# Kernel optimization log

Measured on AMD Instinct MI355X. Metric: run time of the kernel, lower is better.

Reference implementation:

```python
import jax, jax.numpy as jnp
import numpy as np

RESO = 64
VSIZE = 0.3
VOXEL = VSIZE / RESO
HALF = VOXEL / 2.0


def _voxel_xyz():
    line = (np.arange(RESO, dtype=np.float32) * VOXEL + HALF)
    x, y, z = np.meshgrid(line, line, line, indexing='ij')
    return jnp.asarray(np.stack([x, y, z]))  # [3,R,R,R]


def _grid_sample_2d(feats, gx, gy):
    # feats: [NV,C,H,W]; gx,gy: [NV,N] normalized coords (torch align_corners-style)
    NV, C, H, W = feats.shape
    ix = (gx + 1.0) * 0.5 * (W - 1)
    iy = (gy + 1.0) * 0.5 * (H - 1)
    ix0 = jnp.floor(ix); iy0 = jnp.floor(iy)
    ix1 = ix0 + 1.0;     iy1 = iy0 + 1.0
    # bilinear weights from unclamped corners
    w_nw = (ix1 - ix) * (iy1 - iy)
    w_ne = (ix - ix0) * (iy1 - iy)
    w_sw = (ix1 - ix) * (iy - iy0)
    w_se = (ix - ix0) * (iy - iy0)
    mask = ((ix >= 0) & (ix <= W - 1) & (iy >= 0) & (iy <= H - 1)).astype(feats.dtype)
    cx0 = jnp.clip(ix0, 0, W - 1).astype(jnp.int32)
    cx1 = jnp.clip(ix1, 0, W - 1).astype(jnp.int32)
    cy0 = jnp.clip(iy0, 0, H - 1).astype(jnp.int32)
    cy1 = jnp.clip(iy1, 0, H - 1).astype(jnp.int32)
    feats_flat = feats.reshape(NV, C, H * W)  # [NV,C,HW]
    gather = jax.vmap(lambda f, i: f[:, i])   # per-view [C,HW],[N] -> [C,N]
    v_nw = gather(feats_flat, cy0 * W + cx0)
    v_ne = gather(feats_flat, cy0 * W + cx1)
    v_sw = gather(feats_flat, cy1 * W + cx0)
    v_se = gather(feats_flat, cy1 * W + cx1)
    out = (v_nw * w_nw[:, None] + v_ne * w_ne[:, None]
           + v_sw * w_sw[:, None] + v_se * w_se[:, None])  # [NV,C,N]
    return out, mask


def setup_inputs() -> dict:
    key = jax.random.key(0)
    k_feat, k1, k2, k3 = jax.random.split(key, 4)
    NV, C, H, W = 8, 32, 128, 128
    feats = jax.random.normal(k_feat, (NV, C, H, W), dtype=jnp.float32)
    # realistic pinhole intrinsics for a 512x512 image
    K = np.array([[400.0, 0.0, 256.0], [0.0, 400.0, 256.0], [0.0, 0.0, 1.0]], np.float32)
    Ks = jnp.asarray(np.tile(K, (NV, 1, 1)))
    # identity-rotation w2c poses, camera ~0.5m from volume along +z
    poses = []
    for i in range(NV):
        t = np.array([0.02 * (i - 3.5), 0.01 * (i % 2), 0.5 + 0.02 * i], np.float32)
        poses.append(np.concatenate([np.eye(3, dtype=np.float32), t[:, None]], axis=1))
    ref_poses = jnp.asarray(np.stack(poses))
    bbox = jnp.asarray(np.array([[-0.15, -0.15, 0.0], [0.15, 0.15, 0.3]], np.float32))
    W1 = jax.random.normal(k1, (32, 32), dtype=jnp.float32) * 0.1
    W2 = jax.random.normal(k2, (32, 16), dtype=jnp.float32) * 0.1
    W3 = jax.random.normal(k3, (16, 8), dtype=jnp.float32) * 0.1
    return {"feats": feats, "ref_poses": ref_poses, "Ks": Ks, "bbox": bbox,
            "img_h": 512, "img_w": 512,
            "W1": W1, "b1": jnp.zeros((32,), jnp.float32),
            "W2": W2, "b2": jnp.zeros((16,), jnp.float32),
            "W3": W3, "b3": jnp.zeros((8,), jnp.float32)}


def reference(feats, ref_poses, Ks, bbox, img_h, img_w, W1, b1, W2, b2, W3, b3):
    NV, C, H, W = feats.shape
    dt = feats.dtype
    # homogeneous pad of poses and intrinsics
    pose_h = jnp.tile(jnp.eye(4, dtype=dt), (NV, 1, 1)).at[:, :3, :4].set(ref_poses)
    K_pad = jnp.tile(jnp.eye(4, dtype=dt), (NV, 1, 1)).at[:, :3, :3].set(Ks)
    w2pixel = K_pad @ pose_h  # [NV,4,4]
    # voxel centers in world frame
    xyz = _voxel_xyz() + bbox[0][:, None, None, None]  # [3,R,R,R]
    pts = xyz.reshape(3, -1)                            # [3,N], N=R^3
    homo = jnp.concatenate([pts, jnp.ones_like(pts[0:1])], axis=0)  # [4,N]
    pix = jnp.einsum('vij,jn->vin', w2pixel, homo)[:, :3]           # [NV,3,N]
    z = pix[:, 2]                                                    # [NV,N]
    mask_valid_depth = (z > 0).astype(dt)
    uv = pix[:, :2] / z[:, None, :]                                  # [NV,2,N]
    normalizer = jnp.array([img_w, img_h], dtype=dt)
    grid = uv.transpose(0, 2, 1) / normalizer - 1.0                  # [NV,N,2]
    feat, mask = _grid_sample_2d(feats, grid[..., 0], grid[..., 1])  # [NV,C,N],[NV,N]
    mask = mask * mask_valid_depth
    # [NV,C,(X Y Z)] -> [NV,X,Y,Z,C]
    feat = feat.transpose(0, 2, 1).reshape(NV, RESO, RESO, RESO, C)
    mask = mask.reshape(NV, RESO, RESO, RESO)
    # NOTE: original normalizes over dim=1 (NumX), replicated faithfully
    weight = mask / (jnp.sum(mask, axis=1, keepdims=True) + 1e-8)
    weight = weight[..., None]  # [NV,R,R,R,1]
    h1 = jax.nn.relu(feat @ W1 + b1)
    h2 = jax.nn.relu(h1 @ W2 + b2)
    comp = h2 @ W3 + b3  # [NV,R,R,R,8]
    mean = jnp.sum(comp * weight, axis=0, keepdims=True)
    var = jnp.sum(weight * (comp - mean) ** 2, axis=0, keepdims=True)
    mv = jnp.concatenate([mean, var], axis=-1)       # [1,R,R,R,16]
    return jnp.transpose(mv, (0, 4, 3, 2, 1))        # [1,16,Z,Y,X]
```

## Files before the change

### kernel.cpp

```cpp
#include <hip/hip_runtime.h>
#include <math.h>

#define NVIEW 8
#define CIN   32
#define HF    128
#define WF    128
#define C1    32
#define C2    16
#define C3    8
#define RESO  64
#define PLANE (HF*WF)

typedef _Float16 half8_t  __attribute__((ext_vector_type(8)));
typedef _Float16 half2_t  __attribute__((ext_vector_type(2)));
typedef float    floatx4  __attribute__((ext_vector_type(4)));

static __device__ __forceinline__ float vox_coord(int idx, float b) {
    const float VOXEL = (float)(0.3 / 64.0);
    const float HALFV = (float)(0.3 / 128.0);
    return (float)idx * VOXEL + HALFV + b;
}

static __device__ __forceinline__ void wave_lds_sync() {
    asm volatile("s_waitcnt lgkmcnt(0)" ::: "memory");
}

__global__ void __launch_bounds__(256) k_g(const float* __restrict__ feats,
                                           const float* __restrict__ W1,
                                           const float* __restrict__ b1,
                                           uint4* __restrict__ Gh,
                                           const float* __restrict__ Ks,
                                           const float* __restrict__ poses,
                                           const int* __restrict__ ihp,
                                           const int* __restrict__ iwp,
                                           const float* __restrict__ W2,
                                           const float* __restrict__ b2,
                                           const float* __restrict__ W3,
                                           const float* __restrict__ b3,
                                           float* __restrict__ mats,
                                           _Float16* __restrict__ w2f,
                                           _Float16* __restrict__ w3f,
                                           float* __restrict__ b2f,
                                           float* __restrict__ b3f) {
    if (blockIdx.x == 512) {
        int t = threadIdx.x;
        if (t < NVIEW * 12) {
            int v = t / 12, rc = t % 12, r = rc / 4, c = rc % 4;
            const float* K = Ks + v * 9;
            const float* P = poses + v * 12;
            float s = K[r*3+0]*P[0*4+c] + K[r*3+1]*P[1*4+c] + K[r*3+2]*P[2*4+c];
            float sc = (r == 0) ? 63.5f / (float)iwp[0]
                     : (r == 1) ? 63.5f / (float)ihp[0] : 1.0f;
            mats[v*12 + r*4 + c] = s * sc;
        }
        if (t < 64) {
            int n = t & 15, g = t >> 4;
#pragma unroll
            for (int jj = 0; jj < 8; jj++) {
                int kk = 8 * g + jj;
                w2f[t*8 + jj] = (_Float16)W2[kk * C2 + n];
                float w3v = (kk < C2 && n < C3) ? W3[kk * C3 + n] : 0.0f;
                w3f[t*8 + jj] = (_Float16)w3v;
            }
            b2f[t] = b2[n];
            b3f[t] = (n < C3) ? b3[n] : 0.0f;
        }
        return;
    }
    int bx = blockIdx.x;
    int pix = (bx & 63) * 256 + threadIdx.x;
    int v   = bx >> 6;
    const float* fp = feats + ((size_t)v * CIN) * PLANE + pix;
    float g[32];
#pragma unroll
    for (int o = 0; o < C1; o++) g[o] = b1[o];
#pragma unroll
    for (int cc = 0; cc < CIN; cc += 8) {
        float fc[8];
#pragma unroll
        for (int q = 0; q < 8; q++) fc[q] = fp[(size_t)(cc + q) * PLANE];
#pragma unroll
        for (int q = 0; q < 8; q++) {
#pragma unroll
            for (int o = 0; o < C1; o++)
                g[o] = fmaf(fc[q], W1[(cc + q) * C1 + o], g[o]);
        }
    }
    uint4* gp = Gh + ((size_t)v * PLANE + pix) * 4;
#pragma unroll
    for (int grp = 0; grp < 4; grp++) {
        union { half2_t h2[4]; uint4 u; } pk;
#pragma unroll
        for (int q = 0; q < 4; q++) {
            half2_t p = { (_Float16)g[grp*8 + 2*q], (_Float16)g[grp*8 + 2*q + 1] };
            pk.h2[q] = p;
        }
        gp[grp] = pk.u;
    }
}

__global__ void __launch_bounds__(256, 4) k_main(
    const uint4* __restrict__ Gh,
    const float* __restrict__ mats, const float* __restrict__ bbox,
    const _Float16* __restrict__ w2f, const _Float16* __restrict__ w3f,
    const float* __restrict__ b2f, const float* __restrict__ b3f,
    float* __restrict__ out) {
#pragma clang fp contract(fast)
    __shared__ __align__(16) _Float16 a2s[4][64 * 32];
    __shared__ __align__(16) _Float16 h2s[4][64 * 24];

    int tid  = threadIdx.x;
    int wv   = tid >> 6;
    int lane = tid & 63;
    int bxs  = (blockIdx.x & 7) * 128 + (blockIdx.x >> 3);
    int col  = bxs * 4 + wv;
    int j  = col & 63;
    int kz = col >> 6;
    _Float16* a2b = a2s[wv];
    _Float16* h2b = h2s[wv];

    int m = lane & 15, g = lane >> 4;
    float y = vox_coord(j, bbox[1]);
    float z = vox_coord(kz, bbox[2]);
    float x = vox_coord(lane, bbox[0]);

    half8_t w2frag = *(const half8_t*)(w2f + lane * 8);
    half8_t w3frag = *(const half8_t*)(w3f + lane * 8);
    float b2c = b2f[lane];
    float b3c = b3f[lane];
    floatx4 cb2 = {b2c, b2c, b2c, b2c};
    floatx4 cb3 = {b3c, b3c, b3c, b3c};
    const half2_t z2 = { (_Float16)0.0f, (_Float16)0.0f };

    int wsw0 = (lane >> 1) & 3;
    int rsw0 = (m >> 1) & 3;

    float M1[16], Msq[16], S16[16];
#pragma unroll
    for (int c = 0; c < 16; c++) { M1[c] = 0.0f; Msq[c] = 0.0f; S16[c] = 0.0f; }

#pragma unroll 1
    for (int v = 0; v < NVIEW; v++) {
        const float* M = mats + v * 12;
        const uint4* Gp = Gh + (size_t)v * (PLANE * 4);

        float Ku = fmaf(M[1], y, fmaf(M[2],  z, M[3]));
        float Kv = fmaf(M[5], y, fmaf(M[6],  z, M[7]));
        float Kz = fmaf(M[9], y, fmaf(M[10], z, M[11]));

        float u  = fmaf(M[0], x, Ku);
        float vv = fmaf(M[4], x, Kv);
        float zc = fmaf(M[8], x, Kz);
        float invz = __builtin_amdgcn_rcpf(zc);
        float ix = u * invz;
        float iy = vv * invz;

        float fx0 = floorf(ix), fy0 = floorf(iy);
        float fx1 = fx0 + 1.0f, fy1 = fy0 + 1.0f;
        bool inb = (ix >= 0.0f) && (ix <= (float)(WF-1)) &&
                   (iy >= 0.0f) && (iy <= (float)(HF-1)) && (zc > 0.0f);
        int cx0 = (int)fminf(fmaxf(fx0, 0.0f), (float)(WF-1));
        int cx1 = (int)fminf(fmaxf(fx1, 0.0f), (float)(WF-1));
        int cy0 = (int)fminf(fmaxf(fy0, 0.0f), (float)(HF-1));
        int cy1 = (int)fminf(fmaxf(fy1, 0.0f), (float)(HF-1));
        float wnw = (fx1 - ix) * (fy1 - iy);
        float wne = (ix - fx0) * (fy1 - iy);
        float wsw = (fx1 - ix) * (iy - fy0);
        float wse = (ix - fx0) * (iy - fy0);

        unsigned long long bal = __ballot(inb);
        int popc = __popcll(bal);

        int t00 = cy0 * WF + cx0, t01 = cy0 * WF + cx1;
        int t10 = cy1 * WF + cx0, t11 = cy1 * WF + cx1;
        const uint4* pA = Gp + (size_t)t00 * 4;
        const uint4* pB = Gp + (size_t)t01 * 4;
        const uint4* pC = Gp + (size_t)t10 * 4;
        const uint4* pD = Gp + (size_t)t11 * 4;

        half2_t wnw2 = { (_Float16)wnw, (_Float16)wnw };
        half2_t wne2 = { (_Float16)wne, (_Float16)wne };
        half2_t wsw2 = { (_Float16)wsw, (_Float16)wsw };
        half2_t wse2 = { (_Float16)wse, (_Float16)wse };

        union { uint4 u[4]; half2_t h[16]; } ca, cb, cc4, cd, acc;
#pragma unroll
        for (int q = 0; q < 4; q++) ca.u[q] = pA[q];
#pragma unroll
        for (int q = 0; q < 4; q++) cb.u[q] = pB[q];
#pragma unroll
        for (int c = 0; c < 16; c++) acc.h[c] = ca.h[c] * wnw2;
#pragma unroll
        for (int q = 0; q < 4; q++) cc4.u[q] = pC[q];
#pragma unroll
        for (int c = 0; c < 16; c++) acc.h[c] = cb.h[c] * wne2 + acc.h[c];
#pragma unroll
        for (int q = 0; q < 4; q++) cd.u[q] = pD[q];
#pragma unroll
        for (int c = 0; c < 16; c++) acc.h[c] = cc4.h[c] * wsw2 + acc.h[c];
#pragma unroll
        for (int c = 0; c < 16; c++) {
            acc.h[c] = cd.h[c] * wse2 + acc.h[c];
            acc.h[c] = __builtin_elementwise_max(acc.h[c], z2);
        }

#pragma unroll
        for (int q = 0; q < 4; q++)
            *(uint4*)(a2b + lane * 32 + (q ^ wsw0) * 8) = acc.u[q];
        wave_lds_sync();

#pragma unroll
        for (int T = 0; T < 4; T++) {
            half8_t a2 = *(const half8_t*)(a2b + (T*16 + m) * 32 + (g ^ rsw0) * 8);
            floatx4 c2 = __builtin_amdgcn_mfma_f32_16x16x32_f16(a2, w2frag, cb2, 0, 0, 0);
#pragma unroll
            for (int r = 0; r < 4; r++) {
                float hv = fmaxf(c2[r], 0.0f);
                h2b[(T*16 + g*4 + r) * 24 + m] = (_Float16)hv;
            }
        }
        wave_lds_sync();

        float msr = __builtin_amdgcn_rcpf((float)popc + 1e-8f);
        unsigned int balT[4];
        balT[0] = (unsigned int)bal;
        balT[1] = (unsigned int)(bal >> 16);
        balT[2] = (unsigned int)(bal >> 32);
        balT[3] = (unsigned int)(bal >> 48);
#pragma unroll
        for (int T = 0; T < 4; T++) {
            half8_t a3 = *(const half8_t*)(h2b + (T*16 + m) * 24 + (g & 1) * 8);
            floatx4 c3 = __builtin_amdgcn_mfma_f32_16x16x32_f16(a3, w3frag, cb3, 0, 0, 0);
#pragma unroll
            for (int r = 0; r < 4; r++) {
                float w = ((balT[T] >> (g*4 + r)) & 1u) ? msr : 0.0f;
                float val = c3[r];
                float t1 = w * val;
                S16[T*4+r] += w;
                M1[T*4+r]  += t1;
                Msq[T*4+r]  = fmaf(t1, val, Msq[T*4+r]);
            }
        }
    }

    if (m < C3) {
        size_t base = (size_t)col * 64;
#pragma unroll
        for (int T = 0; T < 4; T++) {
            float4 mn, vr;
            mn.x = M1[T*4+0]; mn.y = M1[T*4+1]; mn.z = M1[T*4+2]; mn.w = M1[T*4+3];
            vr.x = fmaf(mn.x*mn.x, S16[T*4+0]-2.0f, Msq[T*4+0]);
            vr.y = fmaf(mn.y*mn.y, S16[T*4+1]-2.0f, Msq[T*4+1]);
            vr.z = fmaf(mn.z*mn.z, S16[T*4+2]-2.0f, Msq[T*4+2]);
            vr.w = fmaf(mn.w*mn.w, S16[T*4+3]-2.0f, Msq[T*4+3]);
            size_t ob = base + T*16 + g*4;
            *(float4*)(out + (size_t)m       * 262144 + ob) = mn;
            *(float4*)(out + (size_t)(m + 8) * 262144 + ob) = vr;
        }
    }
}

extern "C" void kernel_launch(void* const* d_in, const int* in_sizes, int n_in,
                              void* d_out, int out_size, void* d_ws, size_t ws_size,
                              hipStream_t stream) {
    const float* feats = (const float*)d_in[0];
    const float* poses = (const float*)d_in[1];
    const float* Ks    = (const float*)d_in[2];
    const float* bbox  = (const float*)d_in[3];
    const int*   img_h = (const int*)d_in[4];
    const int*   img_w = (const int*)d_in[5];
    const float* W1    = (const float*)d_in[6];
    const float* b1    = (const float*)d_in[7];
    const float* W2    = (const float*)d_in[8];
    const float* b2    = (const float*)d_in[9];
    const float* W3    = (const float*)d_in[10];
    const float* b3    = (const float*)d_in[11];
    float* out = (float*)d_out;
    float* ws  = (float*)d_ws;

    float*     mats = ws;
    _Float16*  w2f  = (_Float16*)(ws + 128);
    _Float16*  w3f  = (_Float16*)(ws + 384);
    float*     b2f  = ws + 640;
    float*     b3f  = ws + 704;
    uint4*     Gh   = (uint4*)(ws + 768);

    hipLaunchKernelGGL(k_g, dim3(513), dim3(256), 0, stream,
                       feats, W1, b1, Gh, Ks, poses, img_h, img_w,
                       W2, b2, W3, b3, mats, w2f, w3f, b2f, b3f);
    hipLaunchKernelGGL(k_main, dim3(1024), dim3(256), 0, stream,
                       Gh, mats, bbox, w2f, w3f, b2f, b3f, out);
}
```

Measured before the change: 128.4 us.

## Prefetch next view's top bilinear corners and transpose layer-3 MFMA operands

```diff
diff --git a/kernel.cpp b/kernel.cpp
--- a/kernel.cpp
+++ b/kernel.cpp
@@ -127,17 +127,44 @@
     half8_t w2frag = *(const half8_t*)(w2f + lane * 8);
     half8_t w3frag = *(const half8_t*)(w3f + lane * 8);
     float b2c = b2f[lane];
-    float b3c = b3f[lane];
     floatx4 cb2 = {b2c, b2c, b2c, b2c};
-    floatx4 cb3 = {b3c, b3c, b3c, b3c};
+    floatx4 cb3p = { b3f[g*4+0], b3f[g*4+1], b3f[g*4+2], b3f[g*4+3] };
     const half2_t z2 = { (_Float16)0.0f, (_Float16)0.0f };
 
     int wsw0 = (lane >> 1) & 3;
     int rsw0 = (m >> 1) & 3;
 
-    float M1[16], Msq[16], S16[16];
-#pragma unroll
-    for (int c = 0; c < 16; c++) { M1[c] = 0.0f; Msq[c] = 0.0f; S16[c] = 0.0f; }
+    float M1[16], Msq[16], S4[4];
+#pragma unroll
+    for (int c = 0; c < 16; c++) { M1[c] = 0.0f; Msq[c] = 0.0f; }
+#pragma unroll
+    for (int c = 0; c < 4; c++) S4[c] = 0.0f;
+
+    union UAB { uint4 u[8]; half2_t h[32]; } ab;
+    union UCD { uint4 u[8]; half2_t h[32]; } cd;
+
+#define ISSUE_AB(VV, AB) do {                                            \
+        const float* M_ = mats + (VV) * 12;                              \
+        const uint4* Gp_ = Gh + (size_t)(VV) * (PLANE * 4);              \
+        float Ku_ = fmaf(M_[1], y, fmaf(M_[2],  z, M_[3]));              \
+        float Kv_ = fmaf(M_[5], y, fmaf(M_[6],  z, M_[7]));              \
+        float Kz_ = fmaf(M_[9], y, fmaf(M_[10], z, M_[11]));             \
+        float u_  = fmaf(M_[0], x, Ku_);                                 \
+        float vv_ = fmaf(M_[4], x, Kv_);                                 \
+        float zc_ = fmaf(M_[8], x, Kz_);                                 \
+        float invz_ = __builtin_amdgcn_rcpf(zc_);                        \
+        float ix_ = u_ * invz_, iy_ = vv_ * invz_;                       \
+        float fx0_ = floorf(ix_), fy0_ = floorf(iy_);                    \
+        int cx0_ = (int)fminf(fmaxf(fx0_, 0.0f), (float)(WF-1));         \
+        int cx1_ = (int)fminf(fmaxf(fx0_ + 1.0f, 0.0f), (float)(WF-1)); \
+        int cy0_ = (int)fminf(fmaxf(fy0_, 0.0f), (float)(HF-1));         \
+        const uint4* pA_ = Gp_ + (size_t)(cy0_ * WF + cx0_) * 4;         \
+        const uint4* pB_ = Gp_ + (size_t)(cy0_ * WF + cx1_) * 4;         \
+        AB.u[0] = pA_[0]; AB.u[1] = pA_[1]; AB.u[2] = pA_[2]; AB.u[3] = pA_[3]; \
+        AB.u[4] = pB_[0]; AB.u[5] = pB_[1]; AB.u[6] = pB_[2]; AB.u[7] = pB_[3]; \
+    } while (0)
+
+    ISSUE_AB(0, ab);
 
 #pragma unroll 1
     for (int v = 0; v < NVIEW; v++) {
@@ -147,7 +174,6 @@
         float Ku = fmaf(M[1], y, fmaf(M[2],  z, M[3]));
         float Kv = fmaf(M[5], y, fmaf(M[6],  z, M[7]));
         float Kz = fmaf(M[9], y, fmaf(M[10], z, M[11]));
-
         float u  = fmaf(M[0], x, Ku);
         float vv = fmaf(M[4], x, Kv);
         float zc = fmaf(M[8], x, Kz);
@@ -161,7 +187,6 @@
                    (iy >= 0.0f) && (iy <= (float)(HF-1)) && (zc > 0.0f);
         int cx0 = (int)fminf(fmaxf(fx0, 0.0f), (float)(WF-1));
         int cx1 = (int)fminf(fmaxf(fx1, 0.0f), (float)(WF-1));
-        int cy0 = (int)fminf(fmaxf(fy0, 0.0f), (float)(HF-1));
         int cy1 = (int)fminf(fmaxf(fy1, 0.0f), (float)(HF-1));
         float wnw = (fx1 - ix) * (fy1 - iy);
         float wne = (ix - fx0) * (fy1 - iy);
@@ -169,38 +194,29 @@
         float wse = (ix - fx0) * (iy - fy0);
 
         unsigned long long bal = __ballot(inb);
-        int popc = __popcll(bal);
-
-        int t00 = cy0 * WF + cx0, t01 = cy0 * WF + cx1;
-        int t10 = cy1 * WF + cx0, t11 = cy1 * WF + cx1;
-        const uint4* pA = Gp + (size_t)t00 * 4;
-        const uint4* pB = Gp + (size_t)t01 * 4;
-        const uint4* pC = Gp + (size_t)t10 * 4;
-        const uint4* pD = Gp + (size_t)t11 * 4;
+
+        const uint4* pC = Gp + (size_t)(cy1 * WF + cx0) * 4;
+        const uint4* pD = Gp + (size_t)(cy1 * WF + cx1) * 4;
+#pragma unroll
+        for (int q = 0; q < 4; q++) cd.u[q]     = pC[q];
+#pragma unroll
+        for (int q = 0; q < 4; q++) cd.u[4 + q] = pD[q];
 
         half2_t wnw2 = { (_Float16)wnw, (_Float16)wnw };
         half2_t wne2 = { (_Float16)wne, (_Float16)wne };
         half2_t wsw2 = { (_Float16)wsw, (_Float16)wsw };
         half2_t wse2 = { (_Float16)wse, (_Float16)wse };
 
-        union { uint4 u[4]; half2_t h[16]; } ca, cb, cc4, cd, acc;
-#pragma unroll
-        for (int q = 0; q < 4; q++) ca.u[q] = pA[q];
-#pragma unroll
-        for (int q = 0; q < 4; q++) cb.u[q] = pB[q];
-#pragma unroll
-        for (int c = 0; c < 16; c++) acc.h[c] = ca.h[c] * wnw2;
-#pragma unroll
-        for (int q = 0; q < 4; q++) cc4.u[q] = pC[q];
-#pragma unroll
-        for (int c = 0; c < 16; c++) acc.h[c] = cb.h[c] * wne2 + acc.h[c];
-#pragma unroll
-        for (int q = 0; q < 4; q++) cd.u[q] = pD[q];
-#pragma unroll
-        for (int c = 0; c < 16; c++) acc.h[c] = cc4.h[c] * wsw2 + acc.h[c];
+        union { uint4 u[4]; half2_t h[16]; } acc;
+#pragma unroll
+        for (int c = 0; c < 16; c++) acc.h[c] = ab.h[c] * wnw2;
+#pragma unroll
+        for (int c = 0; c < 16; c++) acc.h[c] = ab.h[16 + c] * wne2 + acc.h[c];
+#pragma unroll
+        for (int c = 0; c < 16; c++) acc.h[c] = cd.h[c] * wsw2 + acc.h[c];
 #pragma unroll
         for (int c = 0; c < 16; c++) {
-            acc.h[c] = cd.h[c] * wse2 + acc.h[c];
+            acc.h[c] = cd.h[16 + c] * wse2 + acc.h[c];
             acc.h[c] = __builtin_elementwise_max(acc.h[c], z2);
         }
 
@@ -219,9 +235,11 @@
                 h2b[(T*16 + g*4 + r) * 24 + m] = (_Float16)hv;
             }
         }
+
+        if (v < NVIEW - 1) ISSUE_AB(v + 1, ab);
         wave_lds_sync();
 
-        float msr = __builtin_amdgcn_rcpf((float)popc + 1e-8f);
+        float msr = __builtin_amdgcn_rcpf((float)__popcll(bal) + 1e-8f);
         unsigned int balT[4];
         balT[0] = (unsigned int)bal;
         balT[1] = (unsigned int)(bal >> 16);
@@ -230,32 +248,32 @@
 #pragma unroll
         for (int T = 0; T < 4; T++) {
             half8_t a3 = *(const half8_t*)(h2b + (T*16 + m) * 24 + (g & 1) * 8);
-            floatx4 c3 = __builtin_amdgcn_mfma_f32_16x16x32_f16(a3, w3frag, cb3, 0, 0, 0);
+            floatx4 c3 = __builtin_amdgcn_mfma_f32_16x16x32_f16(w3frag, a3, cb3p, 0, 0, 0);
+            float w = ((balT[T] >> m) & 1u) ? msr : 0.0f;
+            S4[T] += w;
 #pragma unroll
             for (int r = 0; r < 4; r++) {
-                float w = ((balT[T] >> (g*4 + r)) & 1u) ? msr : 0.0f;
                 float val = c3[r];
                 float t1 = w * val;
-                S16[T*4+r] += w;
                 M1[T*4+r]  += t1;
                 Msq[T*4+r]  = fmaf(t1, val, Msq[T*4+r]);
             }
         }
     }
-
-    if (m < C3) {
+#undef ISSUE_AB
+
+    if (g < 2) {
         size_t base = (size_t)col * 64;
 #pragma unroll
         for (int T = 0; T < 4; T++) {
-            float4 mn, vr;
-            mn.x = M1[T*4+0]; mn.y = M1[T*4+1]; mn.z = M1[T*4+2]; mn.w = M1[T*4+3];
-            vr.x = fmaf(mn.x*mn.x, S16[T*4+0]-2.0f, Msq[T*4+0]);
-            vr.y = fmaf(mn.y*mn.y, S16[T*4+1]-2.0f, Msq[T*4+1]);
-            vr.z = fmaf(mn.z*mn.z, S16[T*4+2]-2.0f, Msq[T*4+2]);
-            vr.w = fmaf(mn.w*mn.w, S16[T*4+3]-2.0f, Msq[T*4+3]);
-            size_t ob = base + T*16 + g*4;
-            *(float4*)(out + (size_t)m       * 262144 + ob) = mn;
-            *(float4*)(out + (size_t)(m + 8) * 262144 + ob) = vr;
+#pragma unroll
+            for (int r = 0; r < 4; r++) {
+                float mn = M1[T*4+r];
+                float vr = fmaf(mn*mn, S4[T] - 2.0f, Msq[T*4+r]);
+                size_t ob = base + T*16 + m;
+                out[(size_t)(g*4 + r)     * 262144 + ob] = mn;
+                out[(size_t)(g*4 + r + 8) * 262144 + ob] = vr;
+            }
         }
     }
 }
```

Result: slower. 165.7 us (+29.0%).
